# Kernel optimization log

Hardware: AMD Instinct MI355X
Metric: run time of the kernel (lower is better)

## Reference

```python
import jax, jax.numpy as jnp
import numpy as np

N_HEAD = 16
WINDOW = 128
CAUSAL = False


def setup_inputs() -> dict:
    key = jax.random.key(0)
    ks = jax.random.split(key, 5)
    B, T, D = 1, 4096, 1024
    x = jax.random.normal(ks[0], (B, T, D), dtype=jnp.float32)
    w_in = jax.random.normal(ks[1], (3 * D, D), dtype=jnp.float32) * 0.02
    b_in = jax.random.normal(ks[2], (3 * D,), dtype=jnp.float32) * 0.02
    w_out = jax.random.normal(ks[3], (D, D), dtype=jnp.float32) * 0.02
    b_out = jax.random.normal(ks[4], (D,), dtype=jnp.float32) * 0.02
    return {"x": x, "w_in": w_in, "b_in": b_in, "w_out": w_out, "b_out": b_out}


def _window_attention(x, w_in, b_in, w_out, b_out):
    B, T, D = x.shape
    H = N_HEAD
    hd = D // H
    scale = 1.0 / jnp.sqrt(jnp.float32(hd))

    # fused in-projection, as in torch nn.MultiheadAttention (y = x @ W^T + b)
    qkv = jnp.einsum('btd,ed->bte', x, w_in) + b_in  # (B, T, 3D)
    q, k, v = jnp.split(qkv, 3, axis=-1)
    # (B, H, T, hd)
    q = q.reshape(B, T, H, hd).transpose(0, 2, 1, 3)
    k = k.reshape(B, T, H, hd).transpose(0, 2, 1, 3)
    v = v.reshape(B, T, H, hd).transpose(0, 2, 1, 3)

    scores = jnp.einsum('bhqd,bhkd->bhqk', q, k) * scale  # (B, H, T, T)

    idx = jnp.arange(T)
    diff = idx[:, None] - idx[None, :]
    if CAUSAL:
        allowed = (diff >= 0) & (diff <= WINDOW)
    else:
        allowed = jnp.abs(diff) <= WINDOW
    NEG = jnp.float32(-1e30)
    scores = jnp.where(allowed[None, None, :, :], scores, NEG)

    attn = jax.nn.softmax(scores, axis=-1)
    ctx = jnp.einsum('bhqk,bhkd->bhqd', attn, v)  # (B, H, T, hd)
    ctx = ctx.transpose(0, 2, 1, 3).reshape(B, T, D)
    out = jnp.einsum('btd,ed->bte', ctx, w_out) + b_out
    return x + out  # residual, as in the module


def reference(x, w_in, b_in, w_out, b_out):
    return _window_attention(x, w_in, b_in, w_out, b_out)
```

## Files before the change

### kernel.cpp

```cpp
#include <hip/hip_runtime.h>

#define T_SEQ 4096
#define DMODEL 1024
#define NHEAD 16
#define HDIM 64
#define WIN 128

typedef __attribute__((ext_vector_type(8))) short bf16x8;
typedef __attribute__((ext_vector_type(4))) float f32x4;
typedef __attribute__((ext_vector_type(4))) unsigned short u16x4;

__device__ __forceinline__ unsigned short f2bf(float f) {
  unsigned int u = __builtin_bit_cast(unsigned int, f);
  return (unsigned short)((u + 0x7fffu + ((u >> 16) & 1u)) >> 16);
}

__device__ __forceinline__ void gload_lds16(const unsigned short* g,
                                            unsigned short* l) {
  __builtin_amdgcn_global_load_lds(
      (const __attribute__((address_space(1))) void*)g,
      (__attribute__((address_space(3))) void*)l, 16, 0, 0);
}

__global__ void convert_all(const float* __restrict__ x,
                            const float* __restrict__ w_in,
                            const float* __restrict__ w_out,
                            unsigned short* __restrict__ x_bf,
                            unsigned short* __restrict__ w_in_bf,
                            unsigned short* __restrict__ w_out_bf) {
  int stride = gridDim.x * blockDim.x;
  int t0 = blockIdx.x * blockDim.x + threadIdx.x;
#define CVT(SRC, DST, N4)                                          \
  for (int i = t0; i < (N4); i += stride) {                        \
    float4 v = reinterpret_cast<const float4*>(SRC)[i];            \
    u16x4 o;                                                       \
    o.x = f2bf(v.x); o.y = f2bf(v.y); o.z = f2bf(v.z); o.w = f2bf(v.w); \
    reinterpret_cast<u16x4*>(DST)[i] = o;                          \
  }
  CVT(x, x_bf, T_SEQ * DMODEL / 4)
  CVT(w_in, w_in_bf, 3 * DMODEL * DMODEL / 4)
  CVT(w_out, w_out_bf, DMODEL * DMODEL / 4)
#undef CVT
}

template <int EPI, int BM, int BN>
__global__ __launch_bounds__(256) void gemm_lds(
    const unsigned short* __restrict__ A,
    const unsigned short* __restrict__ B,
    const float* __restrict__ bias,
    unsigned short* __restrict__ q_buf,
    unsigned short* __restrict__ k_buf,
    unsigned short* __restrict__ vt_buf,
    const float* __restrict__ x_res,
    float* __restrict__ out) {
  const int K = DMODEL;
  constexpr int MR = BM / 32, NR = BN / 32;
  constexpr int AL = BM / 32, BL = BN / 32;
  __shared__ __align__(16) unsigned short As[BM * 64];
  __shared__ __align__(16) unsigned short Bs[BN * 64];

  int tid = threadIdx.x;
  int lane = tid & 63;
  int wave = tid >> 6;
  int wr = wave >> 1, wc = wave & 1;
  int lo = lane & 15, hi = lane >> 4;
  int t0 = blockIdx.y * BM;
  int e0 = blockIdx.x * BN;

  f32x4 acc[MR][NR];
#pragma unroll
  for (int m = 0; m < MR; ++m)
#pragma unroll
    for (int n = 0; n < NR; ++n) acc[m][n] = (f32x4){0.f, 0.f, 0.f, 0.f};

  const unsigned short* Aptr[AL];
  const unsigned short* Bptr[BL];
  unsigned short* ldsA[AL];
  unsigned short* ldsB[BL];
#pragma unroll
  for (int l = 0; l < AL; ++l) {
    int i = l * 256 + tid;
    int row = i >> 3;
    int c8 = (i & 7) ^ (row & 7);
    Aptr[l] = A + (size_t)(t0 + row) * K + c8 * 8;
    ldsA[l] = As + (l * 256 + wave * 64) * 8;
  }
#pragma unroll
  for (int l = 0; l < BL; ++l) {
    int i = l * 256 + tid;
    int row = i >> 3;
    int c8 = (i & 7) ^ (row & 7);
    Bptr[l] = B + (size_t)(e0 + row) * K + c8 * 8;
    ldsB[l] = Bs + (l * 256 + wave * 64) * 8;
  }

  for (int k0 = 0; k0 < K; k0 += 64) {
    __syncthreads();
#pragma unroll
    for (int l = 0; l < AL; ++l) gload_lds16(Aptr[l] + k0, ldsA[l]);
#pragma unroll
    for (int l = 0; l < BL; ++l) gload_lds16(Bptr[l] + k0, ldsB[l]);
    __syncthreads();

#pragma unroll
    for (int ks = 0; ks < 2; ++ks) {
      bf16x8 af[MR], bfr[NR];
#pragma unroll
      for (int m = 0; m < MR; ++m) {
        int row = wr * (BM / 2) + m * 16 + lo;
        af[m] = *reinterpret_cast<const bf16x8*>(
            &As[row * 64 + ((ks * 4 + hi) ^ (row & 7)) * 8]);
      }
#pragma unroll
      for (int n = 0; n < NR; ++n) {
        int row = wc * (BN / 2) + n * 16 + lo;
        bfr[n] = *reinterpret_cast<const bf16x8*>(
            &Bs[row * 64 + ((ks * 4 + hi) ^ (row & 7)) * 8]);
      }
#pragma unroll
      for (int m = 0; m < MR; ++m)
#pragma unroll
        for (int n = 0; n < NR; ++n)
          acc[m][n] = __builtin_amdgcn_mfma_f32_16x16x32_bf16(af[m], bfr[n],
                                                              acc[m][n], 0, 0, 0);
    }
  }

  int t0w = t0 + wr * (BM / 2);
  int e0w = e0 + wc * (BN / 2);
#pragma unroll
  for (int m = 0; m < MR; ++m) {
#pragma unroll
    for (int n = 0; n < NR; ++n) {
      int e = e0w + n * 16 + lo;
      float bv = bias[e];
      if (EPI == 0) {
        int part = e >> 10;
        int h = (e >> 6) & 15;
        int d = e & 63;
        if (part == 2) {
          int t = t0w + m * 16 + hi * 4;
          u16x4 pk;
          pk.x = f2bf(acc[m][n][0] + bv);
          pk.y = f2bf(acc[m][n][1] + bv);
          pk.z = f2bf(acc[m][n][2] + bv);
          pk.w = f2bf(acc[m][n][3] + bv);
          *reinterpret_cast<u16x4*>(&vt_buf[((size_t)(h * HDIM + d)) * T_SEQ + t]) = pk;
        } else {
          unsigned short* dst = (part == 0) ? q_buf : k_buf;
#pragma unroll
          for (int j = 0; j < 4; ++j) {
            int t = t0w + m * 16 + hi * 4 + j;
            dst[((size_t)h * T_SEQ + t) * HDIM + d] = f2bf(acc[m][n][j] + bv);
          }
        }
      } else {
#pragma unroll
        for (int j = 0; j < 4; ++j) {
          int t = t0w + m * 16 + hi * 4 + j;
          size_t idx = (size_t)t * DMODEL + e;
          out[idx] = acc[m][n][j] + bv + x_res[idx];
        }
      }
    }
  }
}

__global__ __launch_bounds__(256) void win_attn(
    const unsigned short* __restrict__ q_buf,
    const unsigned short* __restrict__ k_buf,
    const unsigned short* __restrict__ vt_buf,
    unsigned short* __restrict__ ctx) {
  __shared__ __align__(16) unsigned short p_lds[4][2][16 * 40];
  int tid = threadIdx.x;
  int wave = tid >> 6;
  int lane = tid & 63;
  int lo = lane & 15, hi = lane >> 4;

  int id = blockIdx.x;
  int sw = (id & 7) * (512 / 8) + (id >> 3);
  int job = sw * 4 + wave;
  int h = job >> 7;
  int q0 = (job & 127) * 32;
  const float SC = 0.18033688011112042f;

  bf16x8 aq[2][2];
#pragma unroll
  for (int u = 0; u < 2; ++u) {
    const unsigned short* qrow =
        q_buf + ((size_t)h * T_SEQ + q0 + u * 16 + lo) * HDIM + hi * 8;
    aq[u][0] = *reinterpret_cast<const bf16x8*>(qrow);
    aq[u][1] = *reinterpret_cast<const bf16x8*>(qrow + 32);
  }

  float L[2][4] = {{0.f, 0.f, 0.f, 0.f}, {0.f, 0.f, 0.f, 0.f}};
  f32x4 o[2][4];
#pragma unroll
  for (int u = 0; u < 2; ++u)
#pragma unroll
    for (int n = 0; n < 4; ++n) o[u][n] = (f32x4){0.f, 0.f, 0.f, 0.f};

  int jstart = q0 - WIN; if (jstart < 0) jstart = 0;
  int jend = q0 + 32 + WIN; if (jend > T_SEQ) jend = T_SEQ;

  bf16x8 kc[2][2];
#pragma unroll
  for (int c = 0; c < 2; ++c) {
    const unsigned short* kp =
        k_buf + ((size_t)h * T_SEQ + jstart + c * 16 + lo) * HDIM + hi * 8;
    kc[c][0] = *reinterpret_cast<const bf16x8*>(kp);
    kc[c][1] = *reinterpret_cast<const bf16x8*>(kp + 32);
  }

  for (int j0 = jstart; j0 < jend; j0 += 32) {
    int jn = (j0 + 32 < jend) ? j0 + 32 : jstart;
    bf16x8 kn[2][2];
#pragma unroll
    for (int c = 0; c < 2; ++c) {
      const unsigned short* kp =
          k_buf + ((size_t)h * T_SEQ + jn + c * 16 + lo) * HDIM + hi * 8;
      kn[c][0] = *reinterpret_cast<const bf16x8*>(kp);
      kn[c][1] = *reinterpret_cast<const bf16x8*>(kp + 32);
    }
    bf16x8 bv[4];
#pragma unroll
    for (int n = 0; n < 4; ++n)
      bv[n] = *reinterpret_cast<const bf16x8*>(
          vt_buf + ((size_t)(h * HDIM + n * 16 + lo)) * T_SEQ + j0 + hi * 8);
#pragma unroll
    for (int u = 0; u < 2; ++u) {
#pragma unroll
      for (int c = 0; c < 2; ++c) {
        f32x4 z = (f32x4){0.f, 0.f, 0.f, 0.f};
        z = __builtin_amdgcn_mfma_f32_16x16x32_bf16(aq[u][0], kc[c][0], z, 0, 0, 0);
        z = __builtin_amdgcn_mfma_f32_16x16x32_bf16(aq[u][1], kc[c][1], z, 0, 0, 0);
        int kj = j0 + c * 16 + lo;
#pragma unroll
        for (int j = 0; j < 4; ++j) {
          int q = q0 + u * 16 + hi * 4 + j;
          bool ok = (q - kj <= WIN) && (kj - q <= WIN);
          float p = ok ? __builtin_amdgcn_exp2f(z[j] * SC) : 0.f;
          L[u][j] += p;
          p_lds[wave][u][(hi * 4 + j) * 40 + c * 16 + lo] = f2bf(p);
        }
      }
    }
    bf16x8 pa[2];
    pa[0] = *reinterpret_cast<const bf16x8*>(&p_lds[wave][0][lo * 40 + hi * 8]);
    pa[1] = *reinterpret_cast<const bf16x8*>(&p_lds[wave][1][lo * 40 + hi * 8]);
#pragma unroll
    for (int n = 0; n < 4; ++n) {
      o[0][n] = __builtin_amdgcn_mfma_f32_16x16x32_bf16(pa[0], bv[n], o[0][n], 0, 0, 0);
      o[1][n] = __builtin_amdgcn_mfma_f32_16x16x32_bf16(pa[1], bv[n], o[1][n], 0, 0, 0);
    }
#pragma unroll
    for (int c = 0; c < 2; ++c) {
      kc[c][0] = kn[c][0];
      kc[c][1] = kn[c][1];
    }
  }
#pragma unroll
  for (int u = 0; u < 2; ++u)
#pragma unroll
    for (int j = 0; j < 4; ++j) {
#pragma unroll
      for (int w = 1; w < 16; w <<= 1) L[u][j] += __shfl_xor(L[u][j], w, 64);
    }
#pragma unroll
  for (int u = 0; u < 2; ++u)
#pragma unroll
    for (int j = 0; j < 4; ++j) {
      int t = q0 + u * 16 + hi * 4 + j;
      float inv = 1.f / L[u][j];
#pragma unroll
      for (int n = 0; n < 4; ++n)
        ctx[(size_t)t * DMODEL + h * HDIM + n * 16 + lo] = f2bf(o[u][n][j] * inv);
    }
}

extern "C" void kernel_launch(void* const* d_in, const int* in_sizes, int n_in,
                              void* d_out, int out_size, void* d_ws, size_t ws_size,
                              hipStream_t stream) {
  const float* x = (const float*)d_in[0];
  const float* w_in = (const float*)d_in[1];
  const float* b_in = (const float*)d_in[2];
  const float* w_out = (const float*)d_in[3];
  const float* b_out = (const float*)d_in[4];
  float* out = (float*)d_out;

  char* ws = (char*)d_ws;
  size_t off = 0;
  auto take = [&](size_t bytes) {
    char* p = ws + off;
    off += (bytes + 255) & ~(size_t)255;
    return p;
  };
  unsigned short* x_bf = (unsigned short*)take((size_t)T_SEQ * DMODEL * 2);
  unsigned short* w_in_bf = (unsigned short*)take((size_t)3 * DMODEL * DMODEL * 2);
  unsigned short* w_out_bf = (unsigned short*)take((size_t)DMODEL * DMODEL * 2);
  unsigned short* q_buf = (unsigned short*)take((size_t)T_SEQ * DMODEL * 2);
  unsigned short* k_buf = (unsigned short*)take((size_t)T_SEQ * DMODEL * 2);
  unsigned short* vt_buf = (unsigned short*)take((size_t)T_SEQ * DMODEL * 2 + 8192);
  unsigned short* ctx = (unsigned short*)take((size_t)T_SEQ * DMODEL * 2);

  convert_all<<<2048, 256, 0, stream>>>(x, w_in, w_out, x_bf, w_in_bf, w_out_bf);

  dim3 g1(3 * DMODEL / 128, T_SEQ / 128);
  gemm_lds<0, 128, 128><<<g1, 256, 0, stream>>>(x_bf, w_in_bf, b_in, q_buf, k_buf,
                                                vt_buf, nullptr, nullptr);

  win_attn<<<512, 256, 0, stream>>>(q_buf, k_buf, vt_buf, ctx);

  dim3 g2(DMODEL / 64, T_SEQ / 128);
  gemm_lds<1, 128, 64><<<g2, 256, 0, stream>>>(ctx, w_out_bf, b_out, nullptr, nullptr,
                                               nullptr, x, out);
}
```

Before: 93.38 us.

## Double-buffer GEMM LDS tiles and widen QKV projection tile to 192

The GEMM kernel now uses two LDS buffers per operand. The next K-slice is issued via global_load_lds while the current slice is computed, and there is a single waitcnt+barrier per iteration instead of two syncthreads. The QKV in-projection tile is widened from 128x128 to 128x192, giving 16x32=512 blocks instead of 768, with more MFMA work per wave. The cost is doubled LDS use (about 80KB for the 192 variant), which can lower occupancy.

```diff
diff --git a/kernel.cpp b/kernel.cpp
--- a/kernel.cpp
+++ b/kernel.cpp
@@ -44,7 +44,7 @@
 }
 
 template <int EPI, int BM, int BN>
-__global__ __launch_bounds__(256) void gemm_lds(
+__global__ __launch_bounds__(256) void gemm_db(
     const unsigned short* __restrict__ A,
     const unsigned short* __restrict__ B,
     const float* __restrict__ bias,
@@ -54,18 +54,18 @@
     const float* __restrict__ x_res,
     float* __restrict__ out) {
   const int K = DMODEL;
-  constexpr int MR = BM / 32, NR = BN / 32;
+  constexpr int NT = DMODEL / 64;
+  constexpr int SM = BM / 2, SN = BN / 2;
+  constexpr int MR = SM / 16, NR = SN / 16;
   constexpr int AL = BM / 32, BL = BN / 32;
-  __shared__ __align__(16) unsigned short As[BM * 64];
-  __shared__ __align__(16) unsigned short Bs[BN * 64];
+  __shared__ __align__(16) unsigned short As[2 * BM * 64];
+  __shared__ __align__(16) unsigned short Bs[2 * BN * 64];
 
   int tid = threadIdx.x;
-  int lane = tid & 63;
-  int wave = tid >> 6;
+  int lane = tid & 63, wave = tid >> 6;
   int wr = wave >> 1, wc = wave & 1;
   int lo = lane & 15, hi = lane >> 4;
-  int t0 = blockIdx.y * BM;
-  int e0 = blockIdx.x * BN;
+  int t0 = blockIdx.y * BM, e0 = blockIdx.x * BN;
 
   f32x4 acc[MR][NR];
 #pragma unroll
@@ -73,61 +73,62 @@
 #pragma unroll
     for (int n = 0; n < NR; ++n) acc[m][n] = (f32x4){0.f, 0.f, 0.f, 0.f};
 
-  const unsigned short* Aptr[AL];
-  const unsigned short* Bptr[BL];
-  unsigned short* ldsA[AL];
-  unsigned short* ldsB[BL];
-#pragma unroll
-  for (int l = 0; l < AL; ++l) {
-    int i = l * 256 + tid;
-    int row = i >> 3;
-    int c8 = (i & 7) ^ (row & 7);
-    Aptr[l] = A + (size_t)(t0 + row) * K + c8 * 8;
-    ldsA[l] = As + (l * 256 + wave * 64) * 8;
-  }
-#pragma unroll
-  for (int l = 0; l < BL; ++l) {
-    int i = l * 256 + tid;
-    int row = i >> 3;
-    int c8 = (i & 7) ^ (row & 7);
-    Bptr[l] = B + (size_t)(e0 + row) * K + c8 * 8;
-    ldsB[l] = Bs + (l * 256 + wave * 64) * 8;
-  }
-
-  for (int k0 = 0; k0 < K; k0 += 64) {
-    __syncthreads();
-#pragma unroll
-    for (int l = 0; l < AL; ++l) gload_lds16(Aptr[l] + k0, ldsA[l]);
-#pragma unroll
-    for (int l = 0; l < BL; ++l) gload_lds16(Bptr[l] + k0, ldsB[l]);
-    __syncthreads();
-
-#pragma unroll
-    for (int ks = 0; ks < 2; ++ks) {
-      bf16x8 af[MR], bfr[NR];
-#pragma unroll
-      for (int m = 0; m < MR; ++m) {
-        int row = wr * (BM / 2) + m * 16 + lo;
-        af[m] = *reinterpret_cast<const bf16x8*>(
-            &As[row * 64 + ((ks * 4 + hi) ^ (row & 7)) * 8]);
-      }
-#pragma unroll
-      for (int n = 0; n < NR; ++n) {
-        int row = wc * (BN / 2) + n * 16 + lo;
-        bfr[n] = *reinterpret_cast<const bf16x8*>(
-            &Bs[row * 64 + ((ks * 4 + hi) ^ (row & 7)) * 8]);
-      }
+  int c8 = (tid & 7) ^ ((tid >> 3) & 7);
+  int srow = tid >> 3;
+  const unsigned short* AbaseG = A + (size_t)(t0 + srow) * K + c8 * 8;
+  const unsigned short* BbaseG = B + (size_t)(e0 + srow) * K + c8 * 8;
+  unsigned short* ldsAu = As + wave * 512;
+  unsigned short* ldsBu = Bs + wave * 512;
+
+  auto stage = [&](int tt) {
+    int k0 = tt * 64;
+    int ab = (tt & 1) * (BM * 64);
+    int bb = (tt & 1) * (BN * 64);
+#pragma unroll
+    for (int l = 0; l < AL; ++l)
+      gload_lds16(AbaseG + (size_t)l * 32 * K + k0, ldsAu + l * 2048 + ab);
+#pragma unroll
+    for (int l = 0; l < BL; ++l)
+      gload_lds16(BbaseG + (size_t)l * 32 * K + k0, ldsBu + l * 2048 + bb);
+  };
+
+  stage(0);
+  asm volatile("s_waitcnt vmcnt(0) lgkmcnt(0)\n\ts_barrier" ::: "memory");
+
+  for (int t = 0; t < NT; ++t) {
+    if (t + 1 < NT) stage(t + 1);
+    const unsigned short* Ab = As + (t & 1) * (BM * 64);
+    const unsigned short* Bb = Bs + (t & 1) * (BN * 64);
+    bf16x8 af[MR][2], bfr[NR][2];
+#pragma unroll
+    for (int m = 0; m < MR; ++m) {
+      int row = wr * SM + m * 16 + lo;
+#pragma unroll
+      for (int ks = 0; ks < 2; ++ks)
+        af[m][ks] = *reinterpret_cast<const bf16x8*>(
+            &Ab[row * 64 + (((ks << 2) + hi) ^ (row & 7)) * 8]);
+    }
+#pragma unroll
+    for (int n = 0; n < NR; ++n) {
+      int row = wc * SN + n * 16 + lo;
+#pragma unroll
+      for (int ks = 0; ks < 2; ++ks)
+        bfr[n][ks] = *reinterpret_cast<const bf16x8*>(
+            &Bb[row * 64 + (((ks << 2) + hi) ^ (row & 7)) * 8]);
+    }
+#pragma unroll
+    for (int ks = 0; ks < 2; ++ks)
 #pragma unroll
       for (int m = 0; m < MR; ++m)
 #pragma unroll
         for (int n = 0; n < NR; ++n)
-          acc[m][n] = __builtin_amdgcn_mfma_f32_16x16x32_bf16(af[m], bfr[n],
+          acc[m][n] = __builtin_amdgcn_mfma_f32_16x16x32_bf16(af[m][ks], bfr[n][ks],
                                                               acc[m][n], 0, 0, 0);
-    }
-  }
-
-  int t0w = t0 + wr * (BM / 2);
-  int e0w = e0 + wc * (BN / 2);
+    asm volatile("s_waitcnt vmcnt(0) lgkmcnt(0)\n\ts_barrier" ::: "memory");
+  }
+
+  int t0w = t0 + wr * SM;
+  int e0w = e0 + wc * SN;
 #pragma unroll
   for (int m = 0; m < MR; ++m) {
 #pragma unroll
@@ -305,13 +306,13 @@
 
   convert_all<<<2048, 256, 0, stream>>>(x, w_in, w_out, x_bf, w_in_bf, w_out_bf);
 
-  dim3 g1(3 * DMODEL / 128, T_SEQ / 128);
-  gemm_lds<0, 128, 128><<<g1, 256, 0, stream>>>(x_bf, w_in_bf, b_in, q_buf, k_buf,
-                                                vt_buf, nullptr, nullptr);
+  dim3 g1(3 * DMODEL / 192, T_SEQ / 128);
+  gemm_db<0, 128, 192><<<g1, 256, 0, stream>>>(x_bf, w_in_bf, b_in, q_buf, k_buf,
+                                               vt_buf, nullptr, nullptr);
 
   win_attn<<<512, 256, 0, stream>>>(q_buf, k_buf, vt_buf, ctx);
 
   dim3 g2(DMODEL / 64, T_SEQ / 128);
-  gemm_lds<1, 128, 64><<<g2, 256, 0, stream>>>(ctx, w_out_bf, b_out, nullptr, nullptr,
-                                               nullptr, x, out);
-}
+  gemm_db<1, 128, 64><<<g2, 256, 0, stream>>>(ctx, w_out_bf, b_out, nullptr, nullptr,
+                                              nullptr, x, out);
+}
```

Result: faster. 89.20 us (-4.5%).
